# Kernel optimization log

Measured on AMD Instinct MI355X. Metric: run time of the kernel, lower is better.

Reference implementation:

```python
import jax, jax.numpy as jnp
import numpy as np

TEMP = 0.05
MOMENTUM = 0.2
NUM_SAMPLES = 65536
NUM_FEATURES = 256
BATCH = 512
EPS = 1e-12

def _l2norm(x, axis=-1):
    return x / jnp.sqrt(jnp.sum(x * x, axis=axis, keepdims=True) + EPS)

def setup_inputs() -> dict:
    key = jax.random.key(0)
    k1, k2, k3 = jax.random.split(key, 3)
    inputs = _l2norm(jax.random.normal(k1, (BATCH, NUM_FEATURES), dtype=jnp.float32))
    targets = jax.random.randint(k2, (BATCH,), 0, NUM_SAMPLES, dtype=jnp.int32)
    features = _l2norm(jax.random.normal(k3, (NUM_SAMPLES, NUM_FEATURES), dtype=jnp.float32))
    return {"inputs": inputs, "targets": targets, "features": features}

def reference(inputs, targets, features):
    # ClusterMemory forward (mode='CM'): logits = (inputs @ features.T) / temp
    logits = jnp.matmul(inputs, features.T) / TEMP  # [B, num_samples]

    # CM side-effect: sequential per-sample EMA scatter update of the memory bank
    # features[y] = m*features[y] + (1-m)*x; features[y] /= ||features[y]||
    # Order-dependent over the batch (duplicate targets), so use lax.scan.
    def step(feats, xy):
        x, y = xy
        row = MOMENTUM * feats[y] + (1.0 - MOMENTUM) * x
        row = row / jnp.sqrt(jnp.sum(row * row) + EPS)
        return feats.at[y].set(row), None

    new_features, _ = jax.lax.scan(step, features, (inputs, targets))
    return logits, new_features
```

## Files before the change

kernel.cpp:

```cpp
#include <hip/hip_runtime.h>
#include <hip/hip_bf16.h>

#define NSAMP   65536
#define NFEAT   256
#define BATCHSZ 512
#define LOGITS_ELEMS ((size_t)BATCHSZ * NSAMP)

typedef __attribute__((ext_vector_type(4))) float f32x4;
typedef __attribute__((ext_vector_type(8))) short bf16x8;

#define BM 128
#define BN 128
#define BK 64

__device__ inline unsigned short bf16_bits(float x) {
  return __builtin_bit_cast(unsigned short, __float2bfloat16(x));
}

__global__ __launch_bounds__(256, 2)
void cm_gemm_kernel(const float* __restrict__ inputs,
                    const float* __restrict__ features,
                    float* __restrict__ logits,
                    float* __restrict__ newF) {
  __shared__ __align__(16) char smem[4 * BM * BK * 2];

  const int tid    = threadIdx.x;
  const int bidx   = blockIdx.x;
  const int m_tile = bidx & 3;
  const int n_tile = bidx >> 2;
  const int bm0    = m_tile * BM;
  const int bn0    = n_tile * BN;

  const int wave  = tid >> 6;
  const int lane  = tid & 63;
  const int m_off = (wave >> 1) * 64;
  const int n_off = (wave & 1) * 64;

  f32x4 acc[4][4];
  #pragma unroll
  for (int m = 0; m < 4; ++m)
    #pragma unroll
    for (int n = 0; n < 4; ++n) {
      acc[m][n][0] = 0.0f; acc[m][n][1] = 0.0f;
      acc[m][n][2] = 0.0f; acc[m][n][3] = 0.0f;
    }

  const int srow = tid >> 3;
  const int slot = tid & 7;

  for (int ks = 0; ks < 4; ++ks) {
    const int k0 = ks * BK;
    if (ks) __syncthreads();

    #pragma unroll
    for (int s = 0; s < 4; ++s) {
      const int row     = srow + s * 32;
      const int byteoff = row * 128 + ((slot * 16) ^ ((row & 7) << 4));

      {
        const float* g = inputs + (size_t)(bm0 + row) * NFEAT + k0 + slot * 8;
        f32x4 v0 = *(const f32x4*)g;
        f32x4 v1 = *(const f32x4*)(g + 4);
        bf16x8 hi, lo;
        #pragma unroll
        for (int e = 0; e < 8; ++e) {
          float x = (e < 4) ? v0[e & 3] : v1[e & 3];
          unsigned short h = bf16_bits(x);
          float hf = __bfloat162float(__builtin_bit_cast(__hip_bfloat16, h));
          hi[e] = (short)h;
          lo[e] = (short)bf16_bits(x - hf);
        }
        *(bf16x8*)(smem + byteoff)         = hi;
        *(bf16x8*)(smem + 16384 + byteoff) = lo;
      }
      {
        const float* g = features + (size_t)(bn0 + row) * NFEAT + k0 + slot * 8;
        f32x4 v0 = *(const f32x4*)g;
        f32x4 v1 = *(const f32x4*)(g + 4);
        bf16x8 hi, lo;
        #pragma unroll
        for (int e = 0; e < 8; ++e) {
          float x = (e < 4) ? v0[e & 3] : v1[e & 3];
          unsigned short h = bf16_bits(x);
          float hf = __bfloat162float(__builtin_bit_cast(__hip_bfloat16, h));
          hi[e] = (short)h;
          lo[e] = (short)bf16_bits(x - hf);
        }
        *(bf16x8*)(smem + 32768 + byteoff) = hi;
        *(bf16x8*)(smem + 49152 + byteoff) = lo;
        if (m_tile == 0) {
          float* o = newF + (size_t)(bn0 + row) * NFEAT + k0 + slot * 8;
          *(f32x4*)o       = v0;
          *(f32x4*)(o + 4) = v1;
        }
      }
    }
    __syncthreads();

    #pragma unroll
    for (int kc = 0; kc < 2; ++kc) {
      const int kbyte = kc * 64 + ((lane >> 4) << 4);
      const int xr    = (lane & 7) << 4;
      bf16x8 ah[4], al[4], bh[4], bl[4];
      #pragma unroll
      for (int m = 0; m < 4; ++m) {
        const int r   = m_off + m * 16 + (lane & 15);
        const int off = r * 128 + (kbyte ^ xr);
        ah[m] = *(const bf16x8*)(smem + off);
        al[m] = *(const bf16x8*)(smem + 16384 + off);
      }
      #pragma unroll
      for (int n = 0; n < 4; ++n) {
        const int r   = n_off + n * 16 + (lane & 15);
        const int off = r * 128 + (kbyte ^ xr);
        bh[n] = *(const bf16x8*)(smem + 32768 + off);
        bl[n] = *(const bf16x8*)(smem + 49152 + off);
      }
      #pragma unroll
      for (int m = 0; m < 4; ++m)
        #pragma unroll
        for (int n = 0; n < 4; ++n) {
          acc[m][n] = __builtin_amdgcn_mfma_f32_16x16x32_bf16(ah[m], bh[n], acc[m][n], 0, 0, 0);
          acc[m][n] = __builtin_amdgcn_mfma_f32_16x16x32_bf16(al[m], bh[n], acc[m][n], 0, 0, 0);
          acc[m][n] = __builtin_amdgcn_mfma_f32_16x16x32_bf16(ah[m], bl[n], acc[m][n], 0, 0, 0);
        }
    }
  }

  const float scale = 1.0f / 0.05f;
  const int c_col      = bn0 + n_off + (lane & 15);
  const int c_row_base = bm0 + m_off + ((lane >> 4) << 2);
  #pragma unroll
  for (int m = 0; m < 4; ++m) {
    #pragma unroll
    for (int n = 0; n < 4; ++n) {
      f32x4 v = acc[m][n];
      size_t base = (size_t)(c_row_base + m * 16) * NSAMP + (size_t)(c_col + n * 16);
      logits[base]             = v[0] * scale;
      logits[base + NSAMP]     = v[1] * scale;
      logits[base + 2 * NSAMP] = v[2] * scale;
      logits[base + 3 * NSAMP] = v[3] * scale;
    }
  }
}

__global__ __launch_bounds__(64)
void cm_update_kernel(const float* __restrict__ inputs,
                      const int* __restrict__ targets,
                      const float* __restrict__ features,
                      float* __restrict__ newF) {
  const int i    = blockIdx.x;
  const int lane = threadIdx.x;
  const int y    = targets[i];

  unsigned long long m[8];
  #pragma unroll
  for (int c = 0; c < 8; ++c)
    m[c] = __ballot(targets[c * 64 + lane] == y);

  int maxj = -1;
  #pragma unroll
  for (int c = 7; c >= 0; --c)
    if (maxj < 0 && m[c]) maxj = c * 64 + 63 - __clzll(m[c]);
  if (maxj != i) return;

  f32x4 row = *(const f32x4*)(features + (size_t)y * NFEAT + lane * 4);
  for (int c = 0; c < 8; ++c) {
    unsigned long long mm = m[c];
    while (mm) {
      const int b = __builtin_ctzll(mm);
      mm &= mm - 1;
      const int j = c * 64 + b;
      f32x4 x = *(const f32x4*)(inputs + (size_t)j * NFEAT + lane * 4);
      row[0] = 0.2f * row[0] + 0.8f * x[0];
      row[1] = 0.2f * row[1] + 0.8f * x[1];
      row[2] = 0.2f * row[2] + 0.8f * x[2];
      row[3] = 0.2f * row[3] + 0.8f * x[3];
      float p = row[0]*row[0] + row[1]*row[1] + row[2]*row[2] + row[3]*row[3];
      #pragma unroll
      for (int off = 32; off >= 1; off >>= 1)
        p += __shfl_xor(p, off);
      const float inv = 1.0f / sqrtf(p + 1e-12f);
      row[0] *= inv; row[1] *= inv; row[2] *= inv; row[3] *= inv;
    }
  }
  *(f32x4*)(newF + (size_t)y * NFEAT + lane * 4) = row;
}

extern "C" void kernel_launch(void* const* d_in, const int* in_sizes, int n_in,
                              void* d_out, int out_size, void* d_ws, size_t ws_size,
                              hipStream_t stream) {
  const float* inputs   = (const float*)d_in[0];
  const int*   targets  = (const int*)d_in[1];
  const float* features = (const float*)d_in[2];
  float* logits = (float*)d_out;
  float* newF   = (float*)d_out + LOGITS_ELEMS;

  const int grid = (NSAMP / BN) * (BATCHSZ / BM);
  cm_gemm_kernel<<<grid, 256, 0, stream>>>(inputs, features, logits, newF);
  cm_update_kernel<<<BATCHSZ, 64, 0, stream>>>(inputs, targets, features, newF);
}
```

Before: 310.0 us.

## Pre-pack bf16 hi/lo splits to workspace and load tiles directly into LDS

```diff
diff --git a/kernel.cpp b/kernel.cpp
--- a/kernel.cpp
+++ b/kernel.cpp
@@ -13,16 +13,179 @@
 #define BN 128
 #define BK 64
 
+#define B_HI_OFF ((size_t)0)
+#define B_LO_OFF ((size_t)33554432)
+#define A_HI_OFF ((size_t)67108864)
+#define A_LO_OFF ((size_t)67371008)
+#define WS_NEEDED ((size_t)(67371008 + 262144))
+#define CHUNK_BYTES 16384
+
+#define FSLOTS (NSAMP * (NFEAT / 8))
+#define ASLOTS (BATCHSZ * (NFEAT / 8))
+
 __device__ inline unsigned short bf16_bits(float x) {
   return __builtin_bit_cast(unsigned short, __float2bfloat16(x));
 }
 
+#define GLOAD_LDS16(gp, lp)                                         \
+  __builtin_amdgcn_global_load_lds(                                 \
+      (const __attribute__((address_space(1))) void*)(gp),          \
+      (__attribute__((address_space(3))) void*)(lp), 16, 0, 0)
+
+__global__ __launch_bounds__(256)
+void cm_pack_kernel(const float* __restrict__ inputs,
+                    const float* __restrict__ features,
+                    char* __restrict__ ws,
+                    float* __restrict__ newF) {
+  const int idx = blockIdx.x * 256 + threadIdx.x;
+  const float* g;
+  size_t dst_hi, dst_lo;
+  if (idx < FSLOTS) {
+    const int R = idx >> 5, s5 = idx & 31;
+    g = features + (size_t)R * NFEAT + s5 * 8;
+    const int p = R >> 7, r = R & 127, ks = s5 >> 3, slot = s5 & 7;
+    const size_t off = (size_t)(p * 4 + ks) * CHUNK_BYTES +
+                       r * 128 + ((slot * 16) ^ ((r & 7) << 4));
+    dst_hi = B_HI_OFF + off;
+    dst_lo = B_LO_OFF + off;
+    float* o = newF + (size_t)R * NFEAT + s5 * 8;
+    *(f32x4*)o       = *(const f32x4*)g;
+    *(f32x4*)(o + 4) = *(const f32x4*)(g + 4);
+  } else if (idx < FSLOTS + ASLOTS) {
+    const int j = idx - FSLOTS;
+    const int R = j >> 5, s5 = j & 31;
+    g = inputs + (size_t)R * NFEAT + s5 * 8;
+    const int p = R >> 7, r = R & 127, ks = s5 >> 3, slot = s5 & 7;
+    const size_t off = (size_t)(p * 4 + ks) * CHUNK_BYTES +
+                       r * 128 + ((slot * 16) ^ ((r & 7) << 4));
+    dst_hi = A_HI_OFF + off;
+    dst_lo = A_LO_OFF + off;
+  } else {
+    return;
+  }
+  f32x4 v0 = *(const f32x4*)g;
+  f32x4 v1 = *(const f32x4*)(g + 4);
+  bf16x8 hi, lo;
+  #pragma unroll
+  for (int e = 0; e < 8; ++e) {
+    float x = (e < 4) ? v0[e & 3] : v1[e & 3];
+    unsigned short h = bf16_bits(x);
+    float hf = __bfloat162float(__builtin_bit_cast(__hip_bfloat16, h));
+    hi[e] = (short)h;
+    lo[e] = (short)bf16_bits(x - hf);
+  }
+  *(bf16x8*)(ws + dst_hi) = hi;
+  *(bf16x8*)(ws + dst_lo) = lo;
+}
+
+__device__ __forceinline__ void mfma_block(const char* smem, int lane,
+                                           int m_off, int n_off,
+                                           f32x4 acc[4][4]) {
+  #pragma unroll
+  for (int kc = 0; kc < 2; ++kc) {
+    const int kbyte = kc * 64 + ((lane >> 4) << 4);
+    const int xr    = (lane & 7) << 4;
+    bf16x8 ah[4], al[4], bh[4], bl[4];
+    #pragma unroll
+    for (int m = 0; m < 4; ++m) {
+      const int r   = m_off + m * 16 + (lane & 15);
+      const int off = r * 128 + (kbyte ^ xr);
+      ah[m] = *(const bf16x8*)(smem + off);
+      al[m] = *(const bf16x8*)(smem + CHUNK_BYTES + off);
+    }
+    #pragma unroll
+    for (int n = 0; n < 4; ++n) {
+      const int r   = n_off + n * 16 + (lane & 15);
+      const int off = r * 128 + (kbyte ^ xr);
+      bh[n] = *(const bf16x8*)(smem + 2 * CHUNK_BYTES + off);
+      bl[n] = *(const bf16x8*)(smem + 3 * CHUNK_BYTES + off);
+    }
+    #pragma unroll
+    for (int m = 0; m < 4; ++m)
+      #pragma unroll
+      for (int n = 0; n < 4; ++n) {
+        acc[m][n] = __builtin_amdgcn_mfma_f32_16x16x32_bf16(ah[m], bh[n], acc[m][n], 0, 0, 0);
+        acc[m][n] = __builtin_amdgcn_mfma_f32_16x16x32_bf16(al[m], bh[n], acc[m][n], 0, 0, 0);
+        acc[m][n] = __builtin_amdgcn_mfma_f32_16x16x32_bf16(ah[m], bl[n], acc[m][n], 0, 0, 0);
+      }
+  }
+}
+
+__device__ __forceinline__ void gemm_epilogue(float* logits, f32x4 acc[4][4],
+                                              int m_tile, int n_tile,
+                                              int m_off, int n_off, int lane) {
+  const float scale = 20.0f;
+  const int c_col      = n_tile * BN + n_off + (lane & 15);
+  const int c_row_base = m_tile * BM + m_off + ((lane >> 4) << 2);
+  #pragma unroll
+  for (int m = 0; m < 4; ++m) {
+    #pragma unroll
+    for (int n = 0; n < 4; ++n) {
+      f32x4 v = acc[m][n];
+      size_t base = (size_t)(c_row_base + m * 16) * NSAMP + (size_t)(c_col + n * 16);
+      logits[base]             = v[0] * scale;
+      logits[base + NSAMP]     = v[1] * scale;
+      logits[base + 2 * NSAMP] = v[2] * scale;
+      logits[base + 3 * NSAMP] = v[3] * scale;
+    }
+  }
+}
+
 __global__ __launch_bounds__(256, 2)
-void cm_gemm_kernel(const float* __restrict__ inputs,
-                    const float* __restrict__ features,
-                    float* __restrict__ logits,
-                    float* __restrict__ newF) {
-  __shared__ __align__(16) char smem[4 * BM * BK * 2];
+void cm_gemm_kernel(const char* __restrict__ ws,
+                    float* __restrict__ logits) {
+  __shared__ __align__(16) char smem[4 * CHUNK_BYTES];
+
+  const int tid = threadIdx.x;
+  const int bid = blockIdx.x;
+  const int swz    = (bid & 7) * 256 + (bid >> 3);
+  const int m_tile = swz & 3;
+  const int n_tile = swz >> 2;
+
+  const int wave  = tid >> 6;
+  const int lane  = tid & 63;
+  const int m_off = (wave >> 1) * 64;
+  const int n_off = (wave & 1) * 64;
+
+  f32x4 acc[4][4];
+  #pragma unroll
+  for (int m = 0; m < 4; ++m)
+    #pragma unroll
+    for (int n = 0; n < 4; ++n) {
+      acc[m][n][0] = 0.0f; acc[m][n][1] = 0.0f;
+      acc[m][n][2] = 0.0f; acc[m][n][3] = 0.0f;
+    }
+
+  const size_t a_base = (size_t)(m_tile * 4) * CHUNK_BYTES;
+  const size_t b_base = (size_t)(n_tile * 4) * CHUNK_BYTES;
+
+  for (int ks = 0; ks < 4; ++ks) {
+    if (ks) __syncthreads();
+
+    const size_t ac = a_base + (size_t)ks * CHUNK_BYTES;
+    const size_t bc = b_base + (size_t)ks * CHUNK_BYTES;
+    #pragma unroll
+    for (int i = 0; i < 4; ++i) {
+      const size_t t = (size_t)i * 4096 + (size_t)tid * 16;
+      GLOAD_LDS16(ws + A_HI_OFF + ac + t, smem + 0 * CHUNK_BYTES + t);
+      GLOAD_LDS16(ws + A_LO_OFF + ac + t, smem + 1 * CHUNK_BYTES + t);
+      GLOAD_LDS16(ws + B_HI_OFF + bc + t, smem + 2 * CHUNK_BYTES + t);
+      GLOAD_LDS16(ws + B_LO_OFF + bc + t, smem + 3 * CHUNK_BYTES + t);
+    }
+    __syncthreads();
+
+    mfma_block(smem, lane, m_off, n_off, acc);
+  }
+
+  gemm_epilogue(logits, acc, m_tile, n_tile, m_off, n_off, lane);
+}
+
+__global__ __launch_bounds__(256, 2)
+void cm_gemm_fused_kernel(const float* __restrict__ inputs,
+                          const float* __restrict__ features,
+                          float* __restrict__ logits,
+                          float* __restrict__ newF) {
+  __shared__ __align__(16) char smem[4 * CHUNK_BYTES];
 
   const int tid    = threadIdx.x;
   const int bidx   = blockIdx.x;
@@ -56,7 +219,6 @@
     for (int s = 0; s < 4; ++s) {
       const int row     = srow + s * 32;
       const int byteoff = row * 128 + ((slot * 16) ^ ((row & 7) << 4));
-
       {
         const float* g = inputs + (size_t)(bm0 + row) * NFEAT + k0 + slot * 8;
         f32x4 v0 = *(const f32x4*)g;
@@ -70,8 +232,8 @@
           hi[e] = (short)h;
           lo[e] = (short)bf16_bits(x - hf);
         }
-        *(bf16x8*)(smem + byteoff)         = hi;
-        *(bf16x8*)(smem + 16384 + byteoff) = lo;
+        *(bf16x8*)(smem + byteoff)               = hi;
+        *(bf16x8*)(smem + CHUNK_BYTES + byteoff) = lo;
       }
       {
         const float* g = features + (size_t)(bn0 + row) * NFEAT + k0 + slot * 8;
@@ -86,8 +248,8 @@
           hi[e] = (short)h;
           lo[e] = (short)bf16_bits(x - hf);
         }
-        *(bf16x8*)(smem + 32768 + byteoff) = hi;
-        *(bf16x8*)(smem + 49152 + byteoff) = lo;
+        *(bf16x8*)(smem + 2 * CHUNK_BYTES + byteoff) = hi;
+        *(bf16x8*)(smem + 3 * CHUNK_BYTES + byteoff) = lo;
         if (m_tile == 0) {
           float* o = newF + (size_t)(bn0 + row) * NFEAT + k0 + slot * 8;
           *(f32x4*)o       = v0;
@@ -97,51 +259,10 @@
     }
     __syncthreads();
 
-    #pragma unroll
-    for (int kc = 0; kc < 2; ++kc) {
-      const int kbyte = kc * 64 + ((lane >> 4) << 4);
-      const int xr    = (lane & 7) << 4;
-      bf16x8 ah[4], al[4], bh[4], bl[4];
-      #pragma unroll
-      for (int m = 0; m < 4; ++m) {
-        const int r   = m_off + m * 16 + (lane & 15);
-        const int off = r * 128 + (kbyte ^ xr);
-        ah[m] = *(const bf16x8*)(smem + off);
-        al[m] = *(const bf16x8*)(smem + 16384 + off);
-      }
-      #pragma unroll
-      for (int n = 0; n < 4; ++n) {
-        const int r   = n_off + n * 16 + (lane & 15);
-        const int off = r * 128 + (kbyte ^ xr);
-        bh[n] = *(const bf16x8*)(smem + 32768 + off);
-        bl[n] = *(const bf16x8*)(smem + 49152 + off);
-      }
-      #pragma unroll
-      for (int m = 0; m < 4; ++m)
-        #pragma unroll
-        for (int n = 0; n < 4; ++n) {
-          acc[m][n] = __builtin_amdgcn_mfma_f32_16x16x32_bf16(ah[m], bh[n], acc[m][n], 0, 0, 0);
-          acc[m][n] = __builtin_amdgcn_mfma_f32_16x16x32_bf16(al[m], bh[n], acc[m][n], 0, 0, 0);
-          acc[m][n] = __builtin_amdgcn_mfma_f32_16x16x32_bf16(ah[m], bl[n], acc[m][n], 0, 0, 0);
-        }
-    }
-  }
-
-  const float scale = 1.0f / 0.05f;
-  const int c_col      = bn0 + n_off + (lane & 15);
-  const int c_row_base = bm0 + m_off + ((lane >> 4) << 2);
-  #pragma unroll
-  for (int m = 0; m < 4; ++m) {
-    #pragma unroll
-    for (int n = 0; n < 4; ++n) {
-      f32x4 v = acc[m][n];
-      size_t base = (size_t)(c_row_base + m * 16) * NSAMP + (size_t)(c_col + n * 16);
-      logits[base]             = v[0] * scale;
-      logits[base + NSAMP]     = v[1] * scale;
-      logits[base + 2 * NSAMP] = v[2] * scale;
-      logits[base + 3 * NSAMP] = v[3] * scale;
-    }
-  }
+    mfma_block(smem, lane, m_off, n_off, acc);
+  }
+
+  gemm_epilogue(logits, acc, m_tile, n_tile, m_off, n_off, lane);
 }
 
 __global__ __launch_bounds__(64)
@@ -197,6 +318,15 @@
   float* newF   = (float*)d_out + LOGITS_ELEMS;
 
   const int grid = (NSAMP / BN) * (BATCHSZ / BM);
-  cm_gemm_kernel<<<grid, 256, 0, stream>>>(inputs, features, logits, newF);
+
+  if (ws_size >= WS_NEEDED) {
+    char* ws = (char*)d_ws;
+    const int pack_blocks = (FSLOTS + ASLOTS) / 256;
+    cm_pack_kernel<<<pack_blocks, 256, 0, stream>>>(inputs, features, ws, newF);
+    cm_gemm_kernel<<<grid, 256, 0, stream>>>(ws, logits);
+  } else {
+    cm_gemm_fused_kernel<<<grid, 256, 0, stream>>>(inputs, features, logits, newF);
+  }
+
   cm_update_kernel<<<BATCHSZ, 64, 0, stream>>>(inputs, targets, features, newF);
 }
```

Measured after the change: 312.2 us. About the same (+0.7%).
